# Kernel tuning notes

Hardware: AMD Instinct MI355X
Metric: run time of the kernel (lower is better)

## Reference

```python
import jax, jax.numpy as jnp
import numpy as np

PAD = 0  # padding token id; its embedding row is zero (padding_idx)


def setup_inputs() -> dict:
    key = jax.random.key(0)
    k1, k2, k3 = jax.random.split(key, 3)
    HOPS, VOCAB, D = 3, 50257, 128
    B, M, S = 32, 512, 6        # batch, memory slots, tokens per slot
    T, L = 128, 64              # trees per example, tokens per (flattened) tree
    # hop+1 embedding tables, normal(0, 0.1) like the torch init
    C = 0.1 * jax.random.normal(k1, (HOPS + 1, VOCAB, D), dtype=jnp.float32)
    C = C.at[:, PAD].set(0.0)   # padding_idx row = 0
    story = jax.random.randint(k2, (B, M, S), 0, VOCAB, dtype=jnp.int32)
    kb_tokens = jax.random.randint(k3, (B, T, L), 0, VOCAB, dtype=jnp.int32)
    return {"C": C, "story": story, "kb_tokens": kb_tokens}


def reference(C, story, kb_tokens):
    # C: [hops+1, V, D]; story: [B, M, S]; kb_tokens: [B, T, L]
    hops = C.shape[0] - 1
    B = story.shape[0]
    D = C.shape[-1]
    u = jnp.zeros((B, D), dtype=C.dtype)
    for hop in range(hops):
        # key memory: story slots (sum over tokens) + tree memories (sum over
        # all subtree tokens == dfs recursive sum, since PAD embeds to zero)
        m_story_A = jnp.take(C[hop], story, axis=0).sum(axis=2)       # [B,M,D]
        tree_A = jnp.take(C[hop], kb_tokens, axis=0).sum(axis=2)      # [B,T,D]
        m_A = jnp.concatenate([m_story_A, tree_A], axis=1)            # [B,M+T,D]
        prob = jax.nn.softmax(jnp.einsum("bmd,bd->bm", m_A, u), axis=1)
        # value memory with next-hop table
        m_story_C = jnp.take(C[hop + 1], story, axis=0).sum(axis=2)
        tree_C = jnp.take(C[hop + 1], kb_tokens, axis=0).sum(axis=2)
        m_C = jnp.concatenate([m_story_C, tree_C], axis=1)
        o_k = jnp.einsum("bm,bmd->bd", prob, m_C)
        u = u + o_k
    return u
```

## Files before the change

### kernel.cpp

```cpp
#include <hip/hip_runtime.h>
#include <math.h>

constexpr int HOPS  = 3;
constexpr int VOCAB = 50257;
constexpr int DIM   = 128;
constexpr int NB    = 32;
constexpr int NM    = 512;
constexpr int NS    = 6;
constexpr int NT    = 128;
constexpr int NL    = 64;
constexpr int SLOTS = NM + NT;
constexpr size_t TS = (size_t)VOCAB * DIM;
constexpr size_t TABSTRIDE = (size_t)NB * SLOTS * DIM;
constexpr int CHUNKS = SLOTS / 64;


__device__ __forceinline__ void addf4(float4& a, const float4& v) {
    a.x += v.x; a.y += v.y; a.z += v.z; a.w += v.w;
}
__device__ __forceinline__ void halfred(float4& a) {
    a.x += __shfl_xor(a.x, 32); a.y += __shfl_xor(a.y, 32);
    a.z += __shfl_xor(a.z, 32); a.w += __shfl_xor(a.w, 32);
}

__global__ __launch_bounds__(256) void story_gather(
    const float* __restrict__ C, const int* __restrict__ story,
    float* __restrict__ msum)
{
    const int wave = threadIdx.x >> 6, lane = threadIdx.x & 63;
    const int g    = blockIdx.x * 4 + wave;
    const int b    = g >> 9;
    const int slot = g & (NM - 1);
    const int half = lane >> 5, q = lane & 31;

    const int* idx = story + (size_t)g * NS;
    int tok = (lane < NS) ? idx[lane] : 0;

    const float* Cb = C + TS + (size_t)q * 4;
    float4 a0 = {0,0,0,0}, a1 = {0,0,0,0}, a2 = {0,0,0,0};
    #pragma unroll
    for (int i = 0; i < NS / 2; ++i) {
        int s = __shfl(tok, 2 * i + half);
        const float* p = Cb + (size_t)s * DIM;
        addf4(a0, *(const float4*)(p));
        addf4(a1, *(const float4*)(p + TS));
        addf4(a2, *(const float4*)(p + 2 * TS));
    }
    halfred(a0); halfred(a1); halfred(a2);
    if (half == 0) {
        const size_t o = ((size_t)b * SLOTS + slot) * DIM + q * 4;
        *(float4*)(msum + o)                 = a0;
        *(float4*)(msum + o + TABSTRIDE)     = a1;
        *(float4*)(msum + o + 2 * TABSTRIDE) = a2;
    }
}

__global__ __launch_bounds__(256) void tree_gather(
    const float* __restrict__ C, const int* __restrict__ kb,
    float* __restrict__ msum)
{
    const int wave = threadIdx.x >> 6, lane = threadIdx.x & 63;
    const int g  = blockIdx.x;
    const int b  = g >> 7;
    const int tr = g & (NT - 1);
    const int half = lane >> 5, q = lane & 31;

    const int* idx = kb + (size_t)g * NL + wave * 16;
    int tok = (lane < 16) ? idx[lane] : 0;

    const float* Cb = C + TS + (size_t)q * 4;
    float4 a0 = {0,0,0,0}, a1 = {0,0,0,0}, a2 = {0,0,0,0};
    #pragma unroll
    for (int i = 0; i < 8; ++i) {
        int s = __shfl(tok, 2 * i + half);
        const float* p = Cb + (size_t)s * DIM;
        addf4(a0, *(const float4*)(p));
        addf4(a1, *(const float4*)(p + TS));
        addf4(a2, *(const float4*)(p + 2 * TS));
    }
    halfred(a0); halfred(a1); halfred(a2);

    __shared__ float lds[4][3][DIM];
    if (half == 0) {
        *(float4*)(&lds[wave][0][q * 4]) = a0;
        *(float4*)(&lds[wave][1][q * 4]) = a1;
        *(float4*)(&lds[wave][2][q * 4]) = a2;
    }
    __syncthreads();
    const int t = threadIdx.x;
    if (t < DIM) {
        const size_t o = ((size_t)b * SLOTS + NM + tr) * DIM + t;
        #pragma unroll
        for (int tab = 0; tab < 3; ++tab) {
            msum[o + (size_t)tab * TABSTRIDE] =
                lds[0][tab][t] + lds[1][tab][t] + lds[2][tab][t] + lds[3][tab][t];
        }
    }
}

__global__ __launch_bounds__(256) void hop0_uniform(
    const float* __restrict__ msum, float* __restrict__ u)
{
    const int b = blockIdx.x / CHUNKS, chunk = blockIdx.x % CHUNKS;
    const int t = threadIdx.x, d = t & (DIM - 1), sub = t >> 7;
    const float* mC = msum + ((size_t)b * SLOTS + chunk * 64 + sub * 32) * DIM + d;
    float acc = 0.f;
    #pragma unroll
    for (int m = 0; m < 32; ++m) acc += mC[(size_t)m * DIM];
    __shared__ float red[256];
    red[t] = acc;
    __syncthreads();
    if (t < DIM) atomicAdd(&u[b * DIM + d], (red[t] + red[t + 128]) * (1.f / SLOTS));
}

__global__ __launch_bounds__(256) void scores_k(
    const float* __restrict__ msum, const float* __restrict__ u,
    float* __restrict__ sc, int tab)
{
    const int wave = threadIdx.x >> 6, lane = threadIdx.x & 63;
    const int g = blockIdx.x * 4 + wave;
    const int b = g / SLOTS;
    float2 v  = *(const float2*)(msum + (size_t)tab * TABSTRIDE + (size_t)g * DIM + lane * 2);
    float2 uu = *(const float2*)(u + b * DIM + lane * 2);
    float acc = fmaf(v.x, uu.x, v.y * uu.y);
    #pragma unroll
    for (int off = 32; off > 0; off >>= 1) acc += __shfl_xor(acc, off);
    if (lane == 0) sc[g] = acc;
}

__global__ __launch_bounds__(256) void softmax_k(float* __restrict__ sc)
{
    const int b = blockIdx.x, t = threadIdx.x, wv = t >> 6, ln = t & 63;
    float* s = sc + b * SLOTS;
    __shared__ float red[4];

    float v0 = s[t], v1 = s[t + 256];
    float v2 = (t < SLOTS - 512) ? s[t + 512] : -INFINITY;
    float lmax = fmaxf(fmaxf(v0, v1), v2);
    #pragma unroll
    for (int off = 32; off > 0; off >>= 1) lmax = fmaxf(lmax, __shfl_xor(lmax, off));
    if (ln == 0) red[wv] = lmax;
    __syncthreads();
    lmax = fmaxf(fmaxf(red[0], red[1]), fmaxf(red[2], red[3]));
    __syncthreads();

    float e0 = expf(v0 - lmax), e1 = expf(v1 - lmax);
    float e2 = (t < SLOTS - 512) ? expf(v2 - lmax) : 0.f;
    float lsum = e0 + e1 + e2;
    #pragma unroll
    for (int off = 32; off > 0; off >>= 1) lsum += __shfl_xor(lsum, off);
    if (ln == 0) red[wv] = lsum;
    __syncthreads();
    const float inv = 1.0f / (red[0] + red[1] + red[2] + red[3]);

    s[t] = e0 * inv; s[t + 256] = e1 * inv;
    if (t < SLOTS - 512) s[t + 512] = e2 * inv;
}

__global__ __launch_bounds__(256) void weighted_k(
    const float* __restrict__ msum, const float* __restrict__ probs,
    float* __restrict__ u, int tab)
{
    const int b = blockIdx.x / CHUNKS, chunk = blockIdx.x % CHUNKS;
    const int t = threadIdx.x, d = t & (DIM - 1), sub = t >> 7;
    __shared__ float p[64];
    if (t < 64) p[t] = probs[b * SLOTS + chunk * 64 + t];
    __syncthreads();
    const float* mC = msum + (size_t)tab * TABSTRIDE +
                      ((size_t)b * SLOTS + chunk * 64 + sub * 32) * DIM + d;
    float acc = 0.f;
    #pragma unroll
    for (int m = 0; m < 32; ++m) acc = fmaf(p[sub * 32 + m], mC[(size_t)m * DIM], acc);
    __shared__ float red[256];
    red[t] = acc;
    __syncthreads();
    if (t < DIM) atomicAdd(&u[b * DIM + d], red[t] + red[t + 128]);
}

extern "C" void kernel_launch(void* const* d_in, const int* in_sizes, int n_in,
                              void* d_out, int out_size, void* d_ws, size_t ws_size,
                              hipStream_t stream) {
    const float* C     = (const float*)d_in[0];
    const int*   story = (const int*)d_in[1];
    const int*   kb    = (const int*)d_in[2];
    float*       u     = (float*)d_out;
    float*       msum  = (float*)d_ws;
    float*       sc    = msum + 3 * TABSTRIDE;

    hipMemsetAsync(u, 0, (size_t)NB * DIM * sizeof(float), stream);

    story_gather<<<NB * NM / 4, 256, 0, stream>>>(C, story, msum);
    tree_gather<<<NB * NT, 256, 0, stream>>>(C, kb, msum);

    hop0_uniform<<<NB * CHUNKS, 256, 0, stream>>>(msum , u);

    for (int hop = 1; hop < HOPS; ++hop) {
        scores_k<<<NB * SLOTS / 4, 256, 0, stream>>>(msum, u, sc, hop - 1);
        softmax_k<<<NB, 256, 0, stream>>>(sc);
        weighted_k<<<NB * CHUNKS, 256, 0, stream>>>(msum, sc, u, hop);
    }
}
```

Measured before the change: 231.8 us.

## Fuse story/tree gathers and scores+softmax; drop memset and atomics in hop0

```diff
diff --git a/kernel.cpp b/kernel.cpp
--- a/kernel.cpp
+++ b/kernel.cpp
@@ -13,6 +13,8 @@
 constexpr size_t TS = (size_t)VOCAB * DIM;
 constexpr size_t TABSTRIDE = (size_t)NB * SLOTS * DIM;
 constexpr int CHUNKS = SLOTS / 64;
+constexpr int TREE_BLOCKS  = NB * NT / 4;
+constexpr int STORY_BLOCKS = NB * NM / 4;
 
 
 __device__ __forceinline__ void addf4(float4& a, const float4& v) {
@@ -23,120 +25,104 @@
     a.z += __shfl_xor(a.z, 32); a.w += __shfl_xor(a.w, 32);
 }
 
-__global__ __launch_bounds__(256) void story_gather(
+__global__ __launch_bounds__(256) void gather_fused(
     const float* __restrict__ C, const int* __restrict__ story,
-    float* __restrict__ msum)
+    const int* __restrict__ kb, float* __restrict__ msum)
 {
     const int wave = threadIdx.x >> 6, lane = threadIdx.x & 63;
-    const int g    = blockIdx.x * 4 + wave;
-    const int b    = g >> 9;
-    const int slot = g & (NM - 1);
     const int half = lane >> 5, q = lane & 31;
-
-    const int* idx = story + (size_t)g * NS;
-    int tok = (lane < NS) ? idx[lane] : 0;
-
     const float* Cb = C + TS + (size_t)q * 4;
     float4 a0 = {0,0,0,0}, a1 = {0,0,0,0}, a2 = {0,0,0,0};
-    #pragma unroll
-    for (int i = 0; i < NS / 2; ++i) {
-        int s = __shfl(tok, 2 * i + half);
-        const float* p = Cb + (size_t)s * DIM;
-        addf4(a0, *(const float4*)(p));
-        addf4(a1, *(const float4*)(p + TS));
-        addf4(a2, *(const float4*)(p + 2 * TS));
-    }
-    halfred(a0); halfred(a1); halfred(a2);
-    if (half == 0) {
-        const size_t o = ((size_t)b * SLOTS + slot) * DIM + q * 4;
-        *(float4*)(msum + o)                 = a0;
-        *(float4*)(msum + o + TABSTRIDE)     = a1;
-        *(float4*)(msum + o + 2 * TABSTRIDE) = a2;
-    }
-}
 
-__global__ __launch_bounds__(256) void tree_gather(
-    const float* __restrict__ C, const int* __restrict__ kb,
-    float* __restrict__ msum)
-{
-    const int wave = threadIdx.x >> 6, lane = threadIdx.x & 63;
-    const int g  = blockIdx.x;
-    const int b  = g >> 7;
-    const int tr = g & (NT - 1);
-    const int half = lane >> 5, q = lane & 31;
-
-    const int* idx = kb + (size_t)g * NL + wave * 16;
-    int tok = (lane < 16) ? idx[lane] : 0;
-
-    const float* Cb = C + TS + (size_t)q * 4;
-    float4 a0 = {0,0,0,0}, a1 = {0,0,0,0}, a2 = {0,0,0,0};
-    #pragma unroll
-    for (int i = 0; i < 8; ++i) {
-        int s = __shfl(tok, 2 * i + half);
-        const float* p = Cb + (size_t)s * DIM;
-        addf4(a0, *(const float4*)(p));
-        addf4(a1, *(const float4*)(p + TS));
-        addf4(a2, *(const float4*)(p + 2 * TS));
-    }
-    halfred(a0); halfred(a1); halfred(a2);
-
-    __shared__ float lds[4][3][DIM];
-    if (half == 0) {
-        *(float4*)(&lds[wave][0][q * 4]) = a0;
-        *(float4*)(&lds[wave][1][q * 4]) = a1;
-        *(float4*)(&lds[wave][2][q * 4]) = a2;
-    }
-    __syncthreads();
-    const int t = threadIdx.x;
-    if (t < DIM) {
-        const size_t o = ((size_t)b * SLOTS + NM + tr) * DIM + t;
+    if (blockIdx.x < TREE_BLOCKS) {
+        const int g = blockIdx.x * 4 + wave;
+        const int tok = kb[(size_t)g * NL + lane];
+        #pragma unroll 8
+        for (int i = 0; i < NL / 2; ++i) {
+            int s = __shfl(tok, 2 * i + half);
+            const float* p = Cb + (size_t)s * DIM;
+            addf4(a0, *(const float4*)(p));
+            addf4(a1, *(const float4*)(p + TS));
+            addf4(a2, *(const float4*)(p + 2 * TS));
+        }
+        halfred(a0); halfred(a1); halfred(a2);
+        if (half == 0) {
+            const int b = g >> 7, tr = g & (NT - 1);
+            const size_t o = ((size_t)b * SLOTS + NM + tr) * DIM + q * 4;
+            *(float4*)(msum + o)                 = a0;
+            *(float4*)(msum + o + TABSTRIDE)     = a1;
+            *(float4*)(msum + o + 2 * TABSTRIDE) = a2;
+        }
+    } else {
+        const int g = (blockIdx.x - TREE_BLOCKS) * 4 + wave;
+        const int* idx = story + (size_t)g * NS;
+        int tok = (lane < NS) ? idx[lane] : 0;
         #pragma unroll
-        for (int tab = 0; tab < 3; ++tab) {
-            msum[o + (size_t)tab * TABSTRIDE] =
-                lds[0][tab][t] + lds[1][tab][t] + lds[2][tab][t] + lds[3][tab][t];
+        for (int i = 0; i < NS / 2; ++i) {
+            int s = __shfl(tok, 2 * i + half);
+            const float* p = Cb + (size_t)s * DIM;
+            addf4(a0, *(const float4*)(p));
+            addf4(a1, *(const float4*)(p + TS));
+            addf4(a2, *(const float4*)(p + 2 * TS));
+        }
+        halfred(a0); halfred(a1); halfred(a2);
+        if (half == 0) {
+            const int b = g >> 9, slot = g & (NM - 1);
+            const size_t o = ((size_t)b * SLOTS + slot) * DIM + q * 4;
+            *(float4*)(msum + o)                 = a0;
+            *(float4*)(msum + o + TABSTRIDE)     = a1;
+            *(float4*)(msum + o + 2 * TABSTRIDE) = a2;
         }
     }
 }
 
-__global__ __launch_bounds__(256) void hop0_uniform(
+__global__ __launch_bounds__(256) void hop0_k(
     const float* __restrict__ msum, float* __restrict__ u)
 {
-    const int b = blockIdx.x / CHUNKS, chunk = blockIdx.x % CHUNKS;
-    const int t = threadIdx.x, d = t & (DIM - 1), sub = t >> 7;
-    const float* mC = msum + ((size_t)b * SLOTS + chunk * 64 + sub * 32) * DIM + d;
+    const int b = blockIdx.x, t = threadIdx.x, d = t & (DIM - 1), sub = t >> 7;
+    const float* mC = msum + ((size_t)b * SLOTS + sub * (SLOTS / 2)) * DIM + d;
     float acc = 0.f;
-    #pragma unroll
-    for (int m = 0; m < 32; ++m) acc += mC[(size_t)m * DIM];
+    #pragma unroll 16
+    for (int m = 0; m < SLOTS / 2; ++m) acc += mC[(size_t)m * DIM];
     __shared__ float red[256];
     red[t] = acc;
     __syncthreads();
-    if (t < DIM) atomicAdd(&u[b * DIM + d], (red[t] + red[t + 128]) * (1.f / SLOTS));
+    if (t < DIM) u[b * DIM + t] = (red[t] + red[t + 128]) * (1.f / SLOTS);
 }
 
-__global__ __launch_bounds__(256) void scores_k(
+__device__ __forceinline__ float dot128(const float* __restrict__ row,
+                                        const float* __restrict__ u_s)
+{
+    float4 acc = {0.f, 0.f, 0.f, 0.f};
+    #pragma unroll
+    for (int i = 0; i < DIM / 4; ++i) {
+        float4 r  = ((const float4*)row)[i];
+        float4 uu = ((const float4*)u_s)[i];
+        acc.x = fmaf(r.x, uu.x, acc.x);
+        acc.y = fmaf(r.y, uu.y, acc.y);
+        acc.z = fmaf(r.z, uu.z, acc.z);
+        acc.w = fmaf(r.w, uu.w, acc.w);
+    }
+    return (acc.x + acc.y) + (acc.z + acc.w);
+}
+
+__global__ __launch_bounds__(256) void scores_softmax_k(
     const float* __restrict__ msum, const float* __restrict__ u,
     float* __restrict__ sc, int tab)
 {
-    const int wave = threadIdx.x >> 6, lane = threadIdx.x & 63;
-    const int g = blockIdx.x * 4 + wave;
-    const int b = g / SLOTS;
-    float2 v  = *(const float2*)(msum + (size_t)tab * TABSTRIDE + (size_t)g * DIM + lane * 2);
-    float2 uu = *(const float2*)(u + b * DIM + lane * 2);
-    float acc = fmaf(v.x, uu.x, v.y * uu.y);
-    #pragma unroll
-    for (int off = 32; off > 0; off >>= 1) acc += __shfl_xor(acc, off);
-    if (lane == 0) sc[g] = acc;
-}
+    const int b = blockIdx.x, t = threadIdx.x, wv = t >> 6, ln = t & 63;
+    __shared__ float u_s[DIM];
+    __shared__ float red[4];
+    if (t < DIM) u_s[t] = u[b * DIM + t];
+    __syncthreads();
 
-__global__ __launch_bounds__(256) void softmax_k(float* __restrict__ sc)
-{
-    const int b = blockIdx.x, t = threadIdx.x, wv = t >> 6, ln = t & 63;
-    float* s = sc + b * SLOTS;
-    __shared__ float red[4];
+    const float* mA = msum + (size_t)tab * TABSTRIDE + (size_t)b * SLOTS * DIM;
+    float s0 = dot128(mA + (size_t)t * DIM, u_s);
+    float s1 = dot128(mA + (size_t)(t + 256) * DIM, u_s);
+    float s2 = (t < SLOTS - 512) ? dot128(mA + (size_t)(t + 512) * DIM, u_s)
+                                 : -INFINITY;
 
-    float v0 = s[t], v1 = s[t + 256];
-    float v2 = (t < SLOTS - 512) ? s[t + 512] : -INFINITY;
-    float lmax = fmaxf(fmaxf(v0, v1), v2);
+    float lmax = fmaxf(fmaxf(s0, s1), s2);
     #pragma unroll
     for (int off = 32; off > 0; off >>= 1) lmax = fmaxf(lmax, __shfl_xor(lmax, off));
     if (ln == 0) red[wv] = lmax;
@@ -144,8 +130,8 @@
     lmax = fmaxf(fmaxf(red[0], red[1]), fmaxf(red[2], red[3]));
     __syncthreads();
 
-    float e0 = expf(v0 - lmax), e1 = expf(v1 - lmax);
-    float e2 = (t < SLOTS - 512) ? expf(v2 - lmax) : 0.f;
+    float e0 = expf(s0 - lmax), e1 = expf(s1 - lmax);
+    float e2 = (t < SLOTS - 512) ? expf(s2 - lmax) : 0.f;
     float lsum = e0 + e1 + e2;
     #pragma unroll
     for (int off = 32; off > 0; off >>= 1) lsum += __shfl_xor(lsum, off);
@@ -153,7 +139,9 @@
     __syncthreads();
     const float inv = 1.0f / (red[0] + red[1] + red[2] + red[3]);
 
-    s[t] = e0 * inv; s[t + 256] = e1 * inv;
+    float* s = sc + b * SLOTS;
+    s[t] = e0 * inv;
+    s[t + 256] = e1 * inv;
     if (t < SLOTS - 512) s[t + 512] = e2 * inv;
 }
 
@@ -187,16 +175,11 @@
     float*       msum  = (float*)d_ws;
     float*       sc    = msum + 3 * TABSTRIDE;
 
-    hipMemsetAsync(u, 0, (size_t)NB * DIM * sizeof(float), stream);
-
-    story_gather<<<NB * NM / 4, 256, 0, stream>>>(C, story, msum);
-    tree_gather<<<NB * NT, 256, 0, stream>>>(C, kb, msum);
-
-    hop0_uniform<<<NB * CHUNKS, 256, 0, stream>>>(msum , u);
+    gather_fused<<<TREE_BLOCKS + STORY_BLOCKS, 256, 0, stream>>>(C, story, kb, msum);
+    hop0_k<<<NB, 256, 0, stream>>>(msum , u);
 
     for (int hop = 1; hop < HOPS; ++hop) {
-        scores_k<<<NB * SLOTS / 4, 256, 0, stream>>>(msum, u, sc, hop - 1);
-        softmax_k<<<NB, 256, 0, stream>>>(sc);
+        scores_softmax_k<<<NB, 256, 0, stream>>>(msum, u, sc, hop - 1);
         weighted_k<<<NB * CHUNKS, 256, 0, stream>>>(msum, sc, u, hop);
     }
 }
```

After: 240.1 us. +3.6%, slower.
